# Performance work log

Hardware: AMD Instinct MI355X
Metric: run time of the kernel (lower is better)

## Reference

```python
import jax, jax.numpy as jnp
import numpy as np
from jax import lax

EPS = 1e-5
NBIT = 127.0  # 8-bit symmetric: 2^(8-1)-1

def ste_round(x):
    return x + lax.stop_gradient(jnp.round(x) - x)

def quant_act(x, rng_max):
    # symmetric fake-quant of activations with learned per-cluster range
    s = rng_max / NBIT
    xq = jnp.clip(ste_round(x / s), -NBIT, NBIT) * s
    return xq, s

def fold_bn(w, gamma, beta, mean, var):
    std = jnp.sqrt(var + EPS)
    scale = gamma / std
    w_f = w * scale[:, None, None, None]
    b_f = beta - mean * scale
    return w_f, b_f

def quant_weight(w):
    # per-output-channel symmetric quant
    s = jnp.max(jnp.abs(w), axis=(1, 2, 3), keepdims=True) / NBIT
    wq = jnp.clip(ste_round(w / s), -NBIT, NBIT) * s
    return wq, s.reshape(-1)

def conv(x, w, stride=1, groups=1, pad=0):
    return lax.conv_general_dilated(
        x, w, window_strides=(stride, stride),
        padding=((pad, pad), (pad, pad)),
        dimension_numbers=('NCHW', 'OIHW', 'NCHW'),
        feature_group_count=groups)

def setup_inputs() -> dict:
    key = jax.random.key(0)
    ks = jax.random.split(key, 24)
    B, Cin, H, W = 64, 96, 28, 28
    Cmid, Cout, NC = 576, 96, 4
    d = {}
    d['x'] = jax.random.normal(ks[0], (B, Cin, H, W), dtype=jnp.float32)
    # conv1: 1x1 expansion
    d['w1'] = jax.random.normal(ks[1], (Cmid, Cin, 1, 1), jnp.float32) * 0.1
    d['g1'] = jax.random.uniform(ks[2], (Cmid,), minval=0.5, maxval=1.5)
    d['b1'] = jax.random.normal(ks[3], (Cmid,)) * 0.1
    d['m1'] = jax.random.normal(ks[4], (Cmid,)) * 0.1
    d['v1'] = jax.random.uniform(ks[5], (Cmid,), minval=0.5, maxval=1.5)
    # conv2: 3x3 depthwise
    d['w2'] = jax.random.normal(ks[6], (Cmid, 1, 3, 3), jnp.float32) * 0.1
    d['g2'] = jax.random.uniform(ks[7], (Cmid,), minval=0.5, maxval=1.5)
    d['b2'] = jax.random.normal(ks[8], (Cmid,)) * 0.1
    d['m2'] = jax.random.normal(ks[9], (Cmid,)) * 0.1
    d['v2'] = jax.random.uniform(ks[10], (Cmid,), minval=0.5, maxval=1.5)
    # conv3: 1x1 projection
    d['w3'] = jax.random.normal(ks[11], (Cout, Cmid, 1, 1), jnp.float32) * 0.1
    d['g3'] = jax.random.uniform(ks[12], (Cout,), minval=0.5, maxval=1.5)
    d['b3'] = jax.random.normal(ks[13], (Cout,)) * 0.1
    d['m3'] = jax.random.normal(ks[14], (Cout,)) * 0.1
    d['v3'] = jax.random.uniform(ks[15], (Cout,), minval=0.5, maxval=1.5)
    # per-cluster learned activation ranges for the 4 QuantAct modules
    d['r0'] = jax.random.uniform(ks[16], (NC,), minval=2.0, maxval=8.0)
    d['r1'] = jax.random.uniform(ks[17], (NC,), minval=2.0, maxval=8.0)
    d['r2'] = jax.random.uniform(ks[18], (NC,), minval=2.0, maxval=8.0)
    d['r3'] = jax.random.uniform(ks[19], (NC,), minval=2.0, maxval=8.0)
    d['cluster'] = 2
    return d

def reference(x, w1, g1, b1, m1, v1, w2, g2, b2, m2, v2,
              w3, g3, b3, m3, v3, r0, r1, r2, r3, cluster):
    identity = x  # residual path (in==out, stride==1)
    # QuantAct -> conv1 (BN-folded, per-channel quant) -> ReLU6
    xq, s0 = quant_act(x, r0[cluster])
    w1f, bf1 = fold_bn(w1, g1, b1, m1, v1)
    w1q, ws1 = quant_weight(w1f)
    y = conv(xq, w1q) + bf1[None, :, None, None]
    y = jnp.clip(y, 0.0, 6.0)
    # QuantAct1 -> depthwise conv2 -> ReLU6
    yq, s1 = quant_act(y, r1[cluster])
    w2f, bf2 = fold_bn(w2, g2, b2, m2, v2)
    w2q, ws2 = quant_weight(w2f)
    y = conv(yq, w2q, stride=1, groups=w2.shape[0], pad=1) + bf2[None, :, None, None]
    y = jnp.clip(y, 0.0, 6.0)
    # QuantAct2 -> conv3 projection
    yq, s2 = quant_act(y, r2[cluster])
    w3f, bf3 = fold_bn(w3, g3, b3, m3, v3)
    w3q, ws3 = quant_weight(w3f)
    y = conv(yq, w3q) + bf3[None, :, None, None]
    # residual add, then int32 requant
    y = y + identity
    out, s3 = quant_act(y, r3[cluster])
    return out, s3
```

## Files before the change

### kernel.cpp

```cpp
#include <hip/hip_runtime.h>
#include <cstdint>
#include <cstddef>

typedef int   v4i __attribute__((ext_vector_type(4)));
typedef float v4f __attribute__((ext_vector_type(4)));
typedef unsigned int u32;

constexpr int B_   = 64;
constexpr int CIN  = 96;
constexpr int P_   = 784;
constexpr int CMID = 576;
constexpr int COUT = 96;
constexpr int NOUT = B_ * COUT * P_;
constexpr float NBITF = 127.0f;
constexpr float EPSF  = 1e-5f;
constexpr float MAGICF = 12582912.0f;
constexpr int   BIASI  = 0x4B400000;

constexpr int Y1S = 29;

__device__ __forceinline__ int dot3(u32 a, u32 w, int acc) {
#if __has_builtin(__builtin_amdgcn_sdot4)
    return __builtin_amdgcn_sdot4((int)a, (int)w, acc, false);
#else
    return acc + (int)(signed char)(a)        * (int)(signed char)(w)
               + (int)(signed char)(a >> 8)   * (int)(signed char)(w >> 8)
               + (int)(signed char)(a >> 16)  * (int)(signed char)(w >> 16);
#endif
}

__device__ __forceinline__ void tr4(u32 S0, u32 S1, u32 S2, u32 S3, u32 O[4]) {
    u32 u01 = __builtin_amdgcn_perm(S1, S0, 0x05010400u);
    u32 u23 = __builtin_amdgcn_perm(S3, S2, 0x05010400u);
    u32 v01 = __builtin_amdgcn_perm(S1, S0, 0x07030602u);
    u32 v23 = __builtin_amdgcn_perm(S3, S2, 0x07030602u);
    O[0] = __builtin_amdgcn_perm(u23, u01, 0x05040100u);
    O[1] = __builtin_amdgcn_perm(u23, u01, 0x07060302u);
    O[2] = __builtin_amdgcn_perm(v23, v01, 0x05040100u);
    O[3] = __builtin_amdgcn_perm(v23, v01, 0x07060302u);
}

__device__ __forceinline__ u32 pack4(u32 t0, u32 t1, u32 t2, u32 t3) {
    u32 p01 = __builtin_amdgcn_perm(t1, t0, 0x05010400u);
    u32 p23 = __builtin_amdgcn_perm(t3, t2, 0x05010400u);
    return __builtin_amdgcn_perm(p23, p01, 0x05040100u);
}

__global__ __launch_bounds__(256)
void prep_w(const float* __restrict__ w1, const float* __restrict__ g1,
            const float* __restrict__ b1, const float* __restrict__ m1,
            const float* __restrict__ v1,
            const float* __restrict__ w2, const float* __restrict__ g2,
            const float* __restrict__ b2, const float* __restrict__ m2,
            const float* __restrict__ v2,
            const float* __restrict__ w3, const float* __restrict__ g3,
            const float* __restrict__ b3, const float* __restrict__ m3,
            const float* __restrict__ v3,
            const float* __restrict__ r0, const float* __restrict__ r1,
            const float* __restrict__ r2, const int* __restrict__ cluster,
            int8_t* __restrict__ w1qp, float2* __restrict__ e1,
            v4i* __restrict__ w2pk,    float2* __restrict__ e2,
            int8_t* __restrict__ w3qp, float2* __restrict__ e3)
{
    int tid = threadIdx.x;
    int c = cluster[0];
    int lane = tid & 63, wv = tid >> 6;
    int blk = blockIdx.x * 4 + wv;

    const float *w, *g, *bb, *mm, *vv;
    int oc, K, which;
    if (blk < CMID)            { which = 0; w = w1; g = g1; bb = b1; mm = m1; vv = v1; oc = blk;            K = CIN;  }
    else if (blk < 2 * CMID)   { which = 1; w = w2; g = g2; bb = b2; mm = m2; vv = v2; oc = blk - CMID;     K = 9;    }
    else                       { which = 2; w = w3; g = g3; bb = b3; mm = m3; vv = v3; oc = blk - 2 * CMID; K = CMID; }

    float scale = g[oc] / sqrtf(vv[oc] + EPSF);

    float mx = 0.f;
    for (int k = lane; k < K; k += 64)
        mx = fmaxf(mx, fabsf(w[oc * K + k] * scale));
    #pragma unroll
    for (int off = 1; off < 64; off <<= 1)
        mx = fmaxf(mx, __shfl_xor(mx, off));

    float s = mx / NBITF;

    int myq = 0;
    for (int k = lane; k < K; k += 64) {
        float wf = w[oc * K + k] * scale;
        float q  = fminf(fmaxf(rintf(wf / s), -127.f), 127.f);
        if (which == 0)      w1qp[oc * 144 + k] = (int8_t)q;
        else if (which == 1) myq = (int)q;
        else                 w3qp[oc * 592 + k] = (int8_t)q;
    }
    if (which == 0 && lane < 12)
        ((u32*)(w1qp + oc * 144))[24 + lane] = 0u;
    if (which == 1) {
        u32 qq[9];
        #pragma unroll
        for (int t = 0; t < 9; t++) qq[t] = (u32)__shfl(myq, t, 64) & 0xffu;
        if (lane == 0) {
            v4i pk;
            pk[0] = (int)(qq[0] | (qq[1] << 8) | (qq[2] << 16));
            pk[1] = (int)(qq[3] | (qq[4] << 8) | (qq[5] << 16));
            pk[2] = (int)(qq[6] | (qq[7] << 8) | (qq[8] << 16));
            pk[3] = 0;
            w2pk[oc] = pk;
        }
    }
    if (lane == 0) {
        float bf = bb[oc] - mm[oc] * scale;
        float s0 = r0[c] / NBITF, s1 = r1[c] / NBITF, s2 = r2[c] / NBITF;
        if (which == 0) {
            float inv_s1 = NBITF / r1[c];
            e1[oc] = make_float2(s0 * s * inv_s1, bf * inv_s1);
        } else if (which == 1) {
            float inv_s2 = NBITF / r2[c];
            e2[oc] = make_float2(s1 * s * inv_s2, bf * inv_s2);
        } else {
            e3[oc] = make_float2(s2 * s, bf);
        }
    }
}

__global__ __launch_bounds__(256, 3)
void conv123d(const v4i* __restrict__ w1q4,
              const float2* __restrict__ e1,
              const v4i* __restrict__ w2pk, const float2* __restrict__ e2,
              const int8_t* __restrict__ w3qp, const float2* __restrict__ e3,
              const float* __restrict__ x,
              const float* __restrict__ r0,
              const float* __restrict__ r1, const float* __restrict__ r2,
              const float* __restrict__ r3, const int* __restrict__ cluster,
              float* __restrict__ out)
{
    __shared__ v4i xw[7 * 8 * 16];
    __shared__ u32 y1s[4][48 * Y1S];
    __shared__ v4i y2c[12 * 56];

    int tid = threadIdx.x, b = blockIdx.y, rt = blockIdx.x;
    int R0 = 2 * rt;
    int W0 = (R0 - 1) * 28;
    int lane = tid & 63, wv = tid >> 6;
    int n = lane & 15, q4 = lane >> 4;

    int   c      = cluster[0];
    float inv_s0 = NBITF / r0[c];
    int   u1i    = (int)fminf(rintf(6.f * NBITF / r1[c]), 127.f);
    int   u2i    = (int)fminf(rintf(6.f * NBITF / r2[c]), 127.f);
    float s3     = r3[c] / NBITF;
    float inv_s3 = NBITF / r3[c];

    for (int i = tid; i < 2688; i += 256) {
        int nn = i & 15;
        int q  = (i >> 4) & 3;
        int gj = i >> 6;
        int g  = gj % 6, jm = gj / 6;
        int px = min(max(W0 + 16 * jm + nn, 0), P_ - 1);
        const float* xp = x + ((size_t)b * CIN + 16 * g + 4 * q) * P_ + px;
        int qv[4];
        #pragma unroll
        for (int j = 0; j < 4; j++) {
            float xf = xp[j * P_];
            qv[j] = (int)fminf(fmaxf(rintf(xf * inv_s0), -127.f), 127.f);
        }
        u32 t0 = __builtin_amdgcn_perm((u32)qv[1], (u32)qv[0], 0x00000400u);
        u32 t1 = __builtin_amdgcn_perm((u32)qv[3], (u32)qv[2], 0x00000400u);
        ((u32*)xw)[((jm * 8 + g) * 16 + nn) * 4 + q] =
            __builtin_amdgcn_perm(t1, t0, 0x05040100u);
    }
    for (int i = tid; i < 7 * 2 * 16; i += 256) {
        int nn = i & 15, gg = (i >> 4) & 1, jm = i >> 5;
        xw[(jm * 8 + 6 + gg) * 16 + nn] = (v4i){0, 0, 0, 0};
    }

    u32* myY1 = y1s[wv];

    int pxl = wv * 16 + n;
    int pxc = min(pxl, 55);
    const v4i* w34 = (const v4i*)w3qp;
    v4i acc3[6];
    #pragma unroll
    for (int i = 0; i < 6; i++) acc3[i] = (v4i){0, 0, 0, 0};

    __syncthreads();

    for (int ph = 0; ph < 3; ph++) {
        int oc0 = ph * 192 + wv * 48;

        v4i    bw[3][2];
        float2 ee[3];
        #pragma unroll
        for (int jn = 0; jn < 3; jn++) {
            int oc = oc0 + 16 * jn + n;
            bw[jn][0] = w1q4[oc * 9 + q4];
            bw[jn][1] = w1q4[oc * 9 + 4 + q4];
            ee[jn] = e1[oc];
        }
        #pragma unroll
        for (int jm = 0; jm < 7; jm++) {
            v4i af0 = xw[(jm * 8 + q4) * 16 + n];
            v4i af1 = xw[(jm * 8 + 4 + q4) * 16 + n];
            int dw = 4 * jm + q4;
            bool valid = (unsigned)(W0 + 4 * dw) < (unsigned)P_;

            #pragma unroll
            for (int jn = 0; jn < 3; jn++) {
                v4i acc = (v4i){0, 0, 0, 0};
                acc = __builtin_amdgcn_mfma_i32_16x16x64_i8(af0, bw[jn][0], acc, 0, 0, 0);
                acc = __builtin_amdgcn_mfma_i32_16x16x64_i8(af1, bw[jn][1], acc, 0, 0, 0);
                u32 t[4];
                #pragma unroll
                for (int r = 0; r < 4; r++) {
                    float f = fmaf((float)acc[r], ee[jn].x, ee[jn].y) + MAGICF;
                    t[r] = (u32)min(max(__float_as_int(f), BIASI), BIASI + u1i);
                }
                u32 pk = pack4(t[0], t[1], t[2], t[3]);
                myY1[(16 * jn + n) * Y1S + dw] = valid ? pk : 0u;
            }
        }

        #pragma unroll
        for (int p = 0; p < 3; p++) {
            int id   = p * 64 + lane;
            int chl  = id >> 2;
            int orow = (id >> 1) & 1;
            int half = id & 1;
            int ch   = oc0 + chl;
            int rb   = chl * Y1S + orow * 7;
            int wbse = chl * Y1S + orow * 21 + half * 4;

            v4i wpk = w2pk[ch];
            u32 pk0 = (u32)wpk[0], pk1 = (u32)wpk[1], pk2 = (u32)wpk[2];
            float2 e = e2[ch];

            u32 P[3], S[3][4], Q[3];
            #pragma unroll
            for (int i = 0; i < 3; i++) {
                int rbi = rb + 7 * i;
                u32 s0 = myY1[rbi + half * 4 + 0];
                u32 s1 = myY1[rbi + half * 4 + 1];
                u32 s2 = myY1[rbi + half * 4 + 2];
                u32 t3 = myY1[rbi + 3];
                u32 t4 = myY1[rbi + 4];
                S[i][0] = s0; S[i][1] = s1; S[i][2] = s2;
                P[i]    = half ? t3 : 0u;
                S[i][3] = half ? 0u : t3;
                Q[i]    = half ? 0u : t4;
            }

            #pragma unroll
            for (int xq = 0; xq < 4; xq++) {
                u32 M0 = (xq == 0) ? P[0] : S[0][xq - 1];
                u32 M1 = (xq == 0) ? P[1] : S[1][xq - 1];
                u32 M2 = (xq == 0) ? P[2] : S[2][xq - 1];
                u32 D0 = S[0][xq], D1 = S[1][xq], D2 = S[2][xq];
                u32 N0 = (xq == 3) ? Q[0] : S[0][xq + 1];
                u32 N1 = (xq == 3) ? Q[1] : S[1][xq + 1];
                u32 N2 = (xq == 3) ? Q[2] : S[2][xq + 1];

                int a0, a1, a2, a3;
                a0 = dot3(__builtin_amdgcn_alignbyte(D0, M0, 3), pk0, 0);
                a0 = dot3(__builtin_amdgcn_alignbyte(D1, M1, 3), pk1, a0);
                a0 = dot3(__builtin_amdgcn_alignbyte(D2, M2, 3), pk2, a0);
                a1 = dot3(D0, pk0, 0);
                a1 = dot3(D1, pk1, a1);
                a1 = dot3(D2, pk2, a1);
                a2 = dot3(__builtin_amdgcn_alignbyte(N0, D0, 1), pk0, 0);
                a2 = dot3(__builtin_amdgcn_alignbyte(N1, D1, 1), pk1, a2);
                a2 = dot3(__builtin_amdgcn_alignbyte(N2, D2, 1), pk2, a2);
                a3 = dot3(__builtin_amdgcn_alignbyte(N0, D0, 2), pk0, 0);
                a3 = dot3(__builtin_amdgcn_alignbyte(N1, D1, 2), pk1, a3);
                a3 = dot3(__builtin_amdgcn_alignbyte(N2, D2, 2), pk2, a3);

                int aa[4] = {a0, a1, a2, a3};
                u32 tq[4];
                #pragma unroll
                for (int i = 0; i < 4; i++) {
                    float f = fmaf((float)aa[i], e.x, e.y) + MAGICF;
                    tq[i] = (u32)min(max(__float_as_int(f), BIASI), BIASI + u2i);
                }
                if (!half || xq < 3)
                    myY1[wbse + xq] = pack4(tq[0], tq[1], tq[2], tq[3]);
            }
        }

        if (lane < 42) {
            int kgl = lane / 14, d = lane - kgl * 14;
            int off = d + ((d >= 7) ? 14 : 0);
            u32 O[4][4];
            #pragma unroll
            for (int j = 0; j < 4; j++) {
                int ch0 = 16 * kgl + 4 * j;
                tr4(myY1[(ch0 + 0) * Y1S + off], myY1[(ch0 + 1) * Y1S + off],
                    myY1[(ch0 + 2) * Y1S + off], myY1[(ch0 + 3) * Y1S + off], O[j]);
            }
            int kgG = wv * 3 + kgl;
            #pragma unroll
            for (int i = 0; i < 4; i++)
                y2c[kgG * 56 + 4 * d + i] =
                    (v4i){(int)O[0][i], (int)O[1][i], (int)O[2][i], (int)O[3][i]};
        }

        __syncthreads();

        #pragma unroll
        for (int ks = 0; ks < 3; ks++) {
            v4i bfr = y2c[(4 * ks + q4) * 56 + pxc];
            #pragma unroll
            for (int i = 0; i < 6; i++) {
                v4i afr = w34[(i * 16 + n) * 37 + ph * 12 + 4 * ks + q4];
                acc3[i] = __builtin_amdgcn_mfma_i32_16x16x64_i8(afr, bfr, acc3[i], 0, 0, 0);
            }
        }

        if (ph < 2) __syncthreads();
    }

    if (pxl < 56) {
        int px = R0 * 28 + pxl;
        #pragma unroll
        for (int i = 0; i < 6; i++) {
            #pragma unroll
            for (int r = 0; r < 4; r++) {
                int    oc = i * 16 + q4 * 4 + r;
                float2 e  = e3[oc];
                size_t gi = (size_t)(b * COUT + oc) * P_ + px;
                float v  = fmaf((float)acc3[i][r], e.x, e.y) + x[gi];
                float f  = fmaf(v, inv_s3, MAGICF);
                int lvl  = min(max(__float_as_int(f) - BIASI, -127), 127);
                out[gi]  = (float)lvl * s3;
            }
        }
    }
    if (rt == 0 && b == 0 && tid == 0)
        out[NOUT] = s3;
}

extern "C" void kernel_launch(void* const* d_in, const int* in_sizes, int n_in,
                              void* d_out, int out_size, void* d_ws, size_t ws_size,
                              hipStream_t stream)
{
    const float* x  = (const float*)d_in[0];
    const float* w1 = (const float*)d_in[1];
    const float* g1 = (const float*)d_in[2];
    const float* b1 = (const float*)d_in[3];
    const float* m1 = (const float*)d_in[4];
    const float* v1 = (const float*)d_in[5];
    const float* w2 = (const float*)d_in[6];
    const float* g2 = (const float*)d_in[7];
    const float* b2 = (const float*)d_in[8];
    const float* m2 = (const float*)d_in[9];
    const float* v2 = (const float*)d_in[10];
    const float* w3 = (const float*)d_in[11];
    const float* g3 = (const float*)d_in[12];
    const float* b3 = (const float*)d_in[13];
    const float* m3 = (const float*)d_in[14];
    const float* v3 = (const float*)d_in[15];
    const float* r0 = (const float*)d_in[16];
    const float* r1 = (const float*)d_in[17];
    const float* r2 = (const float*)d_in[18];
    const float* r3 = (const float*)d_in[19];
    const int*   cl = (const int*)d_in[20];

    float* out = (float*)d_out;

    char*  ws  = (char*)d_ws;
    size_t off = 0;
    auto carve = [&](size_t bytes) {
        size_t cur = off;
        off = (off + bytes + 255) & ~(size_t)255;
        return (void*)(ws + cur);
    };
    int8_t* w1qp = (int8_t*)carve((size_t)CMID * 144);
    float2* e1   = (float2*)carve((size_t)CMID * 8);
    v4i*    w2pk = (v4i*)carve((size_t)CMID * 16);
    float2* e2   = (float2*)carve((size_t)CMID * 8);
    int8_t* w3qp = (int8_t*)carve((size_t)COUT * 592);
    float2* e3   = (float2*)carve((size_t)COUT * 8);
    (void)ws_size; (void)in_sizes; (void)n_in; (void)out_size;

    prep_w<<<dim3(312), dim3(256), 0, stream>>>(
        w1, g1, b1, m1, v1, w2, g2, b2, m2, v2, w3, g3, b3, m3, v3,
        r0, r1, r2, cl,
        w1qp, e1, w2pk, e2, w3qp, e3);

    conv123d<<<dim3(14, B_), dim3(256), 0, stream>>>(
        (const v4i*)w1qp, e1, w2pk, e2, w3qp, e3,
        x, r0, r1, r2, r3, cl, out);
}
```

Baseline: 163.3 us.

## Process four output rows per block to cut depthwise halo recomputation

```diff
diff --git a/kernel.cpp b/kernel.cpp
--- a/kernel.cpp
+++ b/kernel.cpp
@@ -17,7 +17,7 @@
 constexpr float MAGICF = 12582912.0f;
 constexpr int   BIASI  = 0x4B400000;
 
-constexpr int Y1S = 29;
+constexpr int Y1S = 43;
 
 __device__ __forceinline__ int dot3(u32 a, u32 w, int acc) {
 #if __has_builtin(__builtin_amdgcn_sdot4)
@@ -122,7 +122,7 @@
     }
 }
 
-__global__ __launch_bounds__(256, 3)
+__global__ __launch_bounds__(256, 2)
 void conv123d(const v4i* __restrict__ w1q4,
               const float2* __restrict__ e1,
               const v4i* __restrict__ w2pk, const float2* __restrict__ e2,
@@ -133,12 +133,12 @@
               const float* __restrict__ r3, const int* __restrict__ cluster,
               float* __restrict__ out)
 {
-    __shared__ v4i xw[7 * 8 * 16];
+    __shared__ v4i xw[11 * 8 * 16];
     __shared__ u32 y1s[4][48 * Y1S];
-    __shared__ v4i y2c[12 * 56];
+    __shared__ v4i y2c[12 * 112];
 
     int tid = threadIdx.x, b = blockIdx.y, rt = blockIdx.x;
-    int R0 = 2 * rt;
+    int R0 = 4 * rt;
     int W0 = (R0 - 1) * 28;
     int lane = tid & 63, wv = tid >> 6;
     int n = lane & 15, q4 = lane >> 4;
@@ -150,7 +150,7 @@
     float s3     = r3[c] / NBITF;
     float inv_s3 = NBITF / r3[c];
 
-    for (int i = tid; i < 2688; i += 256) {
+    for (int i = tid; i < 4224; i += 256) {
         int nn = i & 15;
         int q  = (i >> 4) & 3;
         int gj = i >> 6;
@@ -168,19 +168,22 @@
         ((u32*)xw)[((jm * 8 + g) * 16 + nn) * 4 + q] =
             __builtin_amdgcn_perm(t1, t0, 0x05040100u);
     }
-    for (int i = tid; i < 7 * 2 * 16; i += 256) {
+    for (int i = tid; i < 11 * 2 * 16; i += 256) {
         int nn = i & 15, gg = (i >> 4) & 1, jm = i >> 5;
         xw[(jm * 8 + 6 + gg) * 16 + nn] = (v4i){0, 0, 0, 0};
     }
 
     u32* myY1 = y1s[wv];
 
-    int pxl = wv * 16 + n;
-    int pxc = min(pxl, 55);
+    int pxl0 = wv * 32 + n;
+    int pxc0 = min(pxl0, 111);
+    int pxc1 = min(pxl0 + 16, 111);
     const v4i* w34 = (const v4i*)w3qp;
-    v4i acc3[6];
+    v4i acc3[2][6];
     #pragma unroll
-    for (int i = 0; i < 6; i++) acc3[i] = (v4i){0, 0, 0, 0};
+    for (int h = 0; h < 2; h++)
+        #pragma unroll
+        for (int i = 0; i < 6; i++) acc3[h][i] = (v4i){0, 0, 0, 0};
 
     __syncthreads();
 
@@ -197,11 +200,11 @@
             ee[jn] = e1[oc];
         }
         #pragma unroll
-        for (int jm = 0; jm < 7; jm++) {
+        for (int jm = 0; jm < 11; jm++) {
             v4i af0 = xw[(jm * 8 + q4) * 16 + n];
             v4i af1 = xw[(jm * 8 + 4 + q4) * 16 + n];
             int dw = 4 * jm + q4;
-            bool valid = (unsigned)(W0 + 4 * dw) < (unsigned)P_;
+            bool inimg = (unsigned)(W0 + 4 * dw) < (unsigned)P_;
 
             #pragma unroll
             for (int jn = 0; jn < 3; jn++) {
@@ -215,7 +218,8 @@
                     t[r] = (u32)min(max(__float_as_int(f), BIASI), BIASI + u1i);
                 }
                 u32 pk = pack4(t[0], t[1], t[2], t[3]);
-                myY1[(16 * jn + n) * Y1S + dw] = valid ? pk : 0u;
+                if (dw < 42)
+                    myY1[(16 * jn + n) * Y1S + dw] = inimg ? pk : 0u;
             }
         }
 
@@ -223,40 +227,33 @@
         for (int p = 0; p < 3; p++) {
             int id   = p * 64 + lane;
             int chl  = id >> 2;
-            int orow = (id >> 1) & 1;
-            int half = id & 1;
+            int orow = id & 3;
             int ch   = oc0 + chl;
             int rb   = chl * Y1S + orow * 7;
-            int wbse = chl * Y1S + orow * 21 + half * 4;
 
             v4i wpk = w2pk[ch];
             u32 pk0 = (u32)wpk[0], pk1 = (u32)wpk[1], pk2 = (u32)wpk[2];
             float2 e = e2[ch];
 
-            u32 P[3], S[3][4], Q[3];
-            #pragma unroll
-            for (int i = 0; i < 3; i++) {
-                int rbi = rb + 7 * i;
-                u32 s0 = myY1[rbi + half * 4 + 0];
-                u32 s1 = myY1[rbi + half * 4 + 1];
-                u32 s2 = myY1[rbi + half * 4 + 2];
-                u32 t3 = myY1[rbi + 3];
-                u32 t4 = myY1[rbi + 4];
-                S[i][0] = s0; S[i][1] = s1; S[i][2] = s2;
-                P[i]    = half ? t3 : 0u;
-                S[i][3] = half ? 0u : t3;
-                Q[i]    = half ? 0u : t4;
-            }
-
-            #pragma unroll
-            for (int xq = 0; xq < 4; xq++) {
-                u32 M0 = (xq == 0) ? P[0] : S[0][xq - 1];
-                u32 M1 = (xq == 0) ? P[1] : S[1][xq - 1];
-                u32 M2 = (xq == 0) ? P[2] : S[2][xq - 1];
-                u32 D0 = S[0][xq], D1 = S[1][xq], D2 = S[2][xq];
-                u32 N0 = (xq == 3) ? Q[0] : S[0][xq + 1];
-                u32 N1 = (xq == 3) ? Q[1] : S[1][xq + 1];
-                u32 N2 = (xq == 3) ? Q[2] : S[2][xq + 1];
+            u32 W[3][7];
+            #pragma unroll
+            for (int r = 0; r < 3; r++)
+                #pragma unroll
+                for (int w = 0; w < 7; w++)
+                    W[r][w] = myY1[rb + r * 7 + w];
+
+            __builtin_amdgcn_sched_barrier(0);
+
+            u32 outw[7];
+            #pragma unroll
+            for (int xq = 0; xq < 7; xq++) {
+                u32 M0 = xq ? W[0][xq - 1] : 0u;
+                u32 M1 = xq ? W[1][xq - 1] : 0u;
+                u32 M2 = xq ? W[2][xq - 1] : 0u;
+                u32 D0 = W[0][xq], D1 = W[1][xq], D2 = W[2][xq];
+                u32 N0 = (xq < 6) ? W[0][xq + 1] : 0u;
+                u32 N1 = (xq < 6) ? W[1][xq + 1] : 0u;
+                u32 N2 = (xq < 6) ? W[2][xq + 1] : 0u;
 
                 int a0, a1, a2, a3;
                 a0 = dot3(__builtin_amdgcn_alignbyte(D0, M0, 3), pk0, 0);
@@ -279,25 +276,27 @@
                     float f = fmaf((float)aa[i], e.x, e.y) + MAGICF;
                     tq[i] = (u32)min(max(__float_as_int(f), BIASI), BIASI + u2i);
                 }
-                if (!half || xq < 3)
-                    myY1[wbse + xq] = pack4(tq[0], tq[1], tq[2], tq[3]);
-            }
-        }
-
-        if (lane < 42) {
-            int kgl = lane / 14, d = lane - kgl * 14;
-            int off = d + ((d >= 7) ? 14 : 0);
+                outw[xq] = pack4(tq[0], tq[1], tq[2], tq[3]);
+            }
+
+            #pragma unroll
+            for (int xq = 0; xq < 7; xq++)
+                myY1[chl * Y1S + orow * 7 + xq] = outw[xq];
+        }
+
+        for (int u = lane; u < 84; u += 64) {
+            int kgl = u / 28, d = u - kgl * 28;
             u32 O[4][4];
             #pragma unroll
             for (int j = 0; j < 4; j++) {
                 int ch0 = 16 * kgl + 4 * j;
-                tr4(myY1[(ch0 + 0) * Y1S + off], myY1[(ch0 + 1) * Y1S + off],
-                    myY1[(ch0 + 2) * Y1S + off], myY1[(ch0 + 3) * Y1S + off], O[j]);
+                tr4(myY1[(ch0 + 0) * Y1S + d], myY1[(ch0 + 1) * Y1S + d],
+                    myY1[(ch0 + 2) * Y1S + d], myY1[(ch0 + 3) * Y1S + d], O[j]);
             }
             int kgG = wv * 3 + kgl;
             #pragma unroll
             for (int i = 0; i < 4; i++)
-                y2c[kgG * 56 + 4 * d + i] =
+                y2c[kgG * 112 + 4 * d + i] =
                     (v4i){(int)O[0][i], (int)O[1][i], (int)O[2][i], (int)O[3][i]};
         }
 
@@ -305,30 +304,36 @@
 
         #pragma unroll
         for (int ks = 0; ks < 3; ks++) {
-            v4i bfr = y2c[(4 * ks + q4) * 56 + pxc];
+            v4i bfr0 = y2c[(4 * ks + q4) * 112 + pxc0];
+            v4i bfr1 = y2c[(4 * ks + q4) * 112 + pxc1];
             #pragma unroll
             for (int i = 0; i < 6; i++) {
                 v4i afr = w34[(i * 16 + n) * 37 + ph * 12 + 4 * ks + q4];
-                acc3[i] = __builtin_amdgcn_mfma_i32_16x16x64_i8(afr, bfr, acc3[i], 0, 0, 0);
+                acc3[0][i] = __builtin_amdgcn_mfma_i32_16x16x64_i8(afr, bfr0, acc3[0][i], 0, 0, 0);
+                acc3[1][i] = __builtin_amdgcn_mfma_i32_16x16x64_i8(afr, bfr1, acc3[1][i], 0, 0, 0);
             }
         }
 
         if (ph < 2) __syncthreads();
     }
 
-    if (pxl < 56) {
-        int px = R0 * 28 + pxl;
-        #pragma unroll
-        for (int i = 0; i < 6; i++) {
-            #pragma unroll
-            for (int r = 0; r < 4; r++) {
-                int    oc = i * 16 + q4 * 4 + r;
-                float2 e  = e3[oc];
-                size_t gi = (size_t)(b * COUT + oc) * P_ + px;
-                float v  = fmaf((float)acc3[i][r], e.x, e.y) + x[gi];
-                float f  = fmaf(v, inv_s3, MAGICF);
-                int lvl  = min(max(__float_as_int(f) - BIASI, -127), 127);
-                out[gi]  = (float)lvl * s3;
+    #pragma unroll
+    for (int h = 0; h < 2; h++) {
+        int pxl = pxl0 + 16 * h;
+        if (pxl < 112) {
+            int px = R0 * 28 + pxl;
+            #pragma unroll
+            for (int i = 0; i < 6; i++) {
+                #pragma unroll
+                for (int r = 0; r < 4; r++) {
+                    int    oc = i * 16 + q4 * 4 + r;
+                    float2 e  = e3[oc];
+                    size_t gi = (size_t)(b * COUT + oc) * P_ + px;
+                    float v  = fmaf((float)acc3[h][i][r], e.x, e.y) + x[gi];
+                    float f  = fmaf(v, inv_s3, MAGICF);
+                    int lvl  = min(max(__float_as_int(f) - BIASI, -127), 127);
+                    out[gi]  = (float)lvl * s3;
+                }
             }
         }
     }
@@ -384,7 +389,7 @@
         r0, r1, r2, cl,
         w1qp, e1, w2pk, e2, w3qp, e3);
 
-    conv123d<<<dim3(14, B_), dim3(256), 0, stream>>>(
+    conv123d<<<dim3(7, B_), dim3(256), 0, stream>>>(
         (const v4i*)w1qp, e1, w2pk, e2, w3qp, e3,
         x, r0, r1, r2, r3, cl, out);
 }
```

Result: faster. 156.6 us (-4.1%).
